# Kernel optimization log

Hardware: AMD Instinct MI355X
Metric: run time of the kernel (lower is better)

The kernel has to match this reference:

```python
import jax, jax.numpy as jnp
import numpy as np

DIM = 192
HEADS = 6
WIN = 7
N = WIN * WIN            # 49 tokens per window
NW = 64                  # windows per image
B = 64                   # images
BW = NW * B              # 4096 total windows
TABLE = (2 * WIN - 1) ** 2  # 169


def setup_inputs() -> dict:
    key = jax.random.key(0)
    ks = jax.random.split(key, 8)
    x = jax.random.normal(ks[0], (BW, N, DIM), dtype=jnp.float32)
    rpi = jax.random.randint(ks[1], (N, N), 0, TABLE, dtype=jnp.int64)
    # 0 / -100 additive mask (as in shifted-window attention)
    mask = jnp.where(jax.random.uniform(ks[2], (NW, N, N)) < 0.1, -100.0, 0.0).astype(jnp.float32)
    qkv_w = jax.random.normal(ks[3], (3 * DIM, DIM), dtype=jnp.float32) * 0.02
    qkv_b = jnp.zeros((3 * DIM,), dtype=jnp.float32)
    proj_w = jax.random.normal(ks[4], (DIM, DIM), dtype=jnp.float32) * 0.02
    proj_b = jnp.zeros((DIM,), dtype=jnp.float32)
    rpb_table = jax.random.normal(ks[5], (TABLE, HEADS), dtype=jnp.float32) * 0.02
    return {"x": x, "rpi": rpi, "mask": mask, "qkv_w": qkv_w, "qkv_b": qkv_b,
            "proj_w": proj_w, "proj_b": proj_b, "rpb_table": rpb_table}


def reference(x, rpi, mask, qkv_w, qkv_b, proj_w, proj_b, rpb_table):
    b_, n, c = x.shape
    hd = c // HEADS
    scale = hd ** -0.5
    qkv = (x @ qkv_w.T + qkv_b).reshape(b_, n, 3, HEADS, hd)
    qkv = jnp.transpose(qkv, (2, 0, 3, 1, 4))
    q, k, v = qkv[0], qkv[1], qkv[2]
    attn = jnp.einsum('bhnd,bhmd->bhnm', q * scale, k)  # [b_, h, n, n]
    # relative position bias gather: [n, n, h] -> [h, n, n]
    bias = rpb_table[rpi.reshape(-1)].reshape(n, n, HEADS)
    attn = attn + jnp.transpose(bias, (2, 0, 1))[None]
    # additive 0/-inf window mask
    nw = mask.shape[0]
    attn = attn.reshape(b_ // nw, nw, HEADS, n, n) + mask[None, :, None]
    attn = attn.reshape(-1, HEADS, n, n)
    attn = jax.nn.softmax(attn, axis=-1)
    out = jnp.einsum('bhnm,bhmd->bhnd', attn, v)
    out = jnp.transpose(out, (0, 2, 1, 3)).reshape(b_, n, c)
    out = out @ proj_w.T + proj_b
    return out
```

## Files before the change

### kernel.cpp

```cpp
#include <hip/hip_runtime.h>

#define DIM    192
#define HEADS  6
#define NTOK   49
#define NWIN   64

typedef __attribute__((ext_vector_type(8))) short short8;
typedef __attribute__((ext_vector_type(4))) float f32x4;

#define XS 200
#define VS 72
#define SS 65
#define PS 72

#define BIAS_ELEMS (HEADS * NTOK * NTOK)
#define WQKV_SOFF   28864
#define WQKV_ELEMS  (3 * DIM * DIM)
#define WPROJ_SOFF  (WQKV_SOFF + WQKV_ELEMS)
#define WPROJ_ELEMS (DIM * DIM)
#define CMB_BOFF    ((size_t)(WPROJ_SOFF + WPROJ_ELEMS) * 2)
#define CMB_ELEMS   (NWIN * HEADS * NTOK * NTOK)

__device__ __forceinline__ unsigned short f2bf(float f) {
    unsigned int u = __float_as_uint(f);
    u += 0x7FFFu + ((u >> 16) & 1u);
    return (unsigned short)(u >> 16);
}

__global__ void wa_prep_kernel(const int* __restrict__ rpi,
                               const float* __restrict__ rpb,
                               const float* __restrict__ qkv_w,
                               const float* __restrict__ proj_w,
                               const float* __restrict__ maskp,
                               float* __restrict__ bias,
                               unsigned short* __restrict__ wqkv,
                               unsigned short* __restrict__ wproj,
                               float* __restrict__ cmb) {
    __shared__ int is64_s;
    if (threadIdx.x < 64) {
        int z = (rpi[2 * (int)threadIdx.x + 1] == 0) ? 1 : 0;
        unsigned long long b = __ballot(z);
        if (threadIdx.x == 0) is64_s = (__popcll(b) >= 48) ? 1 : 0;
    }
    __syncthreads();
    const int is64 = is64_s;
    const int base3 = BIAS_ELEMS + WQKV_ELEMS + WPROJ_ELEMS;
    const int total = base3 + (cmb ? CMB_ELEMS : 0);
    for (int idx = blockIdx.x * blockDim.x + threadIdx.x; idx < total;
         idx += gridDim.x * blockDim.x) {
        if (idx < BIAS_ELEMS) {
            int h  = idx / (NTOK * NTOK);
            int nm = idx - h * (NTOK * NTOK);
            int r  = is64 ? rpi[2 * nm] : rpi[nm];
            bias[idx] = rpb[r * HEADS + h];
        } else if (idx < BIAS_ELEMS + WQKV_ELEMS) {
            int i = idx - BIAS_ELEMS;
            wqkv[i] = f2bf(qkv_w[i]);
        } else if (idx < base3) {
            int i = idx - BIAS_ELEMS - WQKV_ELEMS;
            wproj[i] = f2bf(proj_w[i]);
        } else {
            int i2  = idx - base3;
            int win = i2 / (HEADS * NTOK * NTOK);
            int rem = i2 - win * (HEADS * NTOK * NTOK);
            int h   = rem / (NTOK * NTOK);
            int nm  = rem - h * (NTOK * NTOK);
            int r   = is64 ? rpi[2 * nm] : rpi[nm];
            cmb[i2] = rpb[r * HEADS + h] + maskp[win * (NTOK * NTOK) + nm];
        }
    }
}

template <bool CMB>
__global__ __launch_bounds__(512, 2)
void wa_attn_kernel(const float* __restrict__ x,
                    const float* __restrict__ maskp,
                    const unsigned short* __restrict__ wqkv,
                    const float* __restrict__ qkv_b,
                    const float* __restrict__ biasp,
                    const unsigned short* __restrict__ wproj,
                    const float* __restrict__ proj_b,
                    const float* __restrict__ cmbp,
                    float* __restrict__ out) {
    __shared__ __attribute__((aligned(16))) float uSP[64 * SS + 64 * (PS / 2)];
    __shared__ __attribute__((aligned(16))) unsigned short sq[64 * XS];
    __shared__ __attribute__((aligned(16))) unsigned short sv[DIM * VS];
    __shared__ float sinv[64];

    unsigned short* sx     = (unsigned short*)uSP;
    unsigned short* kstage = (unsigned short*)uSP;
    float* S = uSP;
    unsigned short* P = (unsigned short*)(uSP + 64 * SS);

    const int tid  = threadIdx.x;
    const int wave = tid >> 6;
    const int lane = tid & 63;
    const int quad = lane >> 4;
    const int l16  = lane & 15;
    const int bw   = blockIdx.x;
    const int win  = bw & (NWIN - 1);

    {
        const float4* xw = (const float4*)(x + (size_t)bw * (NTOK * DIM));
        for (int idx = tid; idx < NTOK * DIM / 4; idx += 512) {
            int row = idx / 48, c4 = idx - row * 48;
            float4 v = xw[idx];
            unsigned int lo = (unsigned int)f2bf(v.x) | ((unsigned int)f2bf(v.y) << 16);
            unsigned int hi = (unsigned int)f2bf(v.z) | ((unsigned int)f2bf(v.w) << 16);
            *(uint2*)&sx[row * XS + c4 * 4] = make_uint2(lo, hi);
        }
        for (int idx = tid; idx < 15 * 24; idx += 512) {
            int row = 49 + idx / 24, c8 = idx - (idx / 24) * 24;
            *(uint4*)&sx[row * XS + c8 * 8] = make_uint4(0, 0, 0, 0);
        }
    }
    __syncthreads();

    {
        f32x4 acc[5][4];
        #pragma unroll
        for (int r = 0; r < 5; ++r)
            #pragma unroll
            for (int mt = 0; mt < 4; ++mt) acc[r][mt] = (f32x4){0.f, 0.f, 0.f, 0.f};
        for (int k0 = 0; k0 < DIM; k0 += 32) {
            short8 af[4];
            #pragma unroll
            for (int mt = 0; mt < 4; ++mt)
                af[mt] = *(const short8*)&sx[(mt * 16 + l16) * XS + k0 + quad * 8];
            #pragma unroll
            for (int r = 0; r < 5; ++r) {
                if (wave >= 4 && r == 4) continue;
                int n0 = (wave + 8 * r) * 16;
                short8 bf = *(const short8*)(wqkv + (n0 + l16) * DIM + k0 + quad * 8);
                #pragma unroll
                for (int mt = 0; mt < 4; ++mt)
                    acc[r][mt] = __builtin_amdgcn_mfma_f32_16x16x32_bf16(af[mt], bf, acc[r][mt], 0, 0, 0);
            }
        }
        __syncthreads();
        #pragma unroll
        for (int r = 0; r < 5; ++r) {
            if (wave >= 4 && r == 4) continue;
            int col = (wave + 8 * r) * 16 + l16;
            float cb = qkv_b[col];
            #pragma unroll
            for (int mt = 0; mt < 4; ++mt) {
                if (r >= 3) {
                    unsigned int lo = (unsigned int)f2bf(acc[r][mt][0] + cb) |
                                      ((unsigned int)f2bf(acc[r][mt][1] + cb) << 16);
                    unsigned int hi = (unsigned int)f2bf(acc[r][mt][2] + cb) |
                                      ((unsigned int)f2bf(acc[r][mt][3] + cb) << 16);
                    *(uint2*)&sv[(col - 384) * VS + mt * 16 + quad * 4] = make_uint2(lo, hi);
                } else {
                    #pragma unroll
                    for (int rr = 0; rr < 4; ++rr) {
                        int m = mt * 16 + quad * 4 + rr;
                        unsigned short bv = f2bf(acc[r][mt][rr] + cb);
                        if (col < 192) sq[m * XS + col] = bv;
                        else           kstage[m * XS + (col - 192)] = bv;
                    }
                }
            }
        }
    }
    __syncthreads();

    short8 kf[2][HEADS];
    #pragma unroll
    for (int tt = 0; tt < 2; ++tt) {
        int t = wave * 2 + tt, nt = t & 3;
        #pragma unroll
        for (int h = 0; h < HEADS; ++h)
            kf[tt][h] = *(const short8*)&kstage[(nt * 16 + l16) * XS + h * 32 + quad * 8];
    }
    __syncthreads();

    const float scale = 0.17677669529663687f;
    const float* maskw = maskp + win * (NTOK * NTOK);

    #pragma unroll
    for (int h = 0; h < HEADS; ++h) {
        {
            f32x4 zz = {0.f, 0.f, 0.f, 0.f};
            const float* cw = CMB ? (cmbp + ((size_t)win * HEADS + h) * (NTOK * NTOK))
                                  : (biasp + h * (NTOK * NTOK));
            #pragma unroll
            for (int tt = 0; tt < 2; ++tt) {
                int t = wave * 2 + tt;
                int mt = t >> 2, nt = t & 3;
                short8 af = *(const short8*)&sq[(mt * 16 + l16) * XS + h * 32 + quad * 8];
                f32x4 d = __builtin_amdgcn_mfma_f32_16x16x32_bf16(af, kf[tt][h], zz, 0, 0, 0);
                #pragma unroll
                for (int rr = 0; rr < 4; ++rr) {
                    int i = mt * 16 + quad * 4 + rr;
                    int j = nt * 16 + l16;
                    if (i < NTOK && j < NTOK) {
                        float add = CMB ? cw[i * NTOK + j]
                                        : (cw[i * NTOK + j] + maskw[i * NTOK + j]);
                        S[i * SS + j] = d[rr] * scale + add;
                    }
                }
            }
        }
        __syncthreads();
        if (tid < 392) {
            int i = tid >> 3, s = tid & 7;
            float m = -1e30f;
            for (int jj = 0; jj < 7; ++jj) {
                int j = s + 8 * jj;
                if (j < NTOK) m = fmaxf(m, S[i * SS + j]);
            }
            for (int o = 1; o < 8; o <<= 1) m = fmaxf(m, __shfl_xor(m, o));
            float sum = 0.f;
            #pragma unroll
            for (int jj = 0; jj < 8; ++jj) {
                int j = s + 8 * jj;
                float e = 0.f;
                if (j < NTOK) { e = __expf(S[i * SS + j] - m); sum += e; }
                P[i * PS + j] = f2bf(e);
            }
            for (int o = 1; o < 8; o <<= 1) sum += __shfl_xor(sum, o);
            if (s == 0) sinv[i] = 1.f / sum;
        }
        __syncthreads();
        {
            int mt = wave >> 1, nt = wave & 1;
            f32x4 acc = {0.f, 0.f, 0.f, 0.f};
            #pragma unroll
            for (int k0 = 0; k0 < 64; k0 += 32) {
                short8 af = *(const short8*)&P[(mt * 16 + l16) * PS + k0 + quad * 8];
                short8 bf = *(const short8*)&sv[(h * 32 + nt * 16 + l16) * VS + k0 + quad * 8];
                acc = __builtin_amdgcn_mfma_f32_16x16x32_bf16(af, bf, acc, 0, 0, 0);
            }
            #pragma unroll
            for (int rr = 0; rr < 4; ++rr) {
                int i = mt * 16 + quad * 4 + rr;
                unsigned short ov = 0;
                if (i < NTOK) ov = f2bf(acc[rr] * sinv[i]);
                sq[i * XS + h * 32 + nt * 16 + l16] = ov;
            }
        }
    }
    __syncthreads();

    {
        const int mh = wave >> 2;
        const int wv = wave & 3;
        f32x4 pacc[3][2];
        #pragma unroll
        for (int r = 0; r < 3; ++r)
            #pragma unroll
            for (int mi = 0; mi < 2; ++mi) pacc[r][mi] = (f32x4){0.f, 0.f, 0.f, 0.f};
        for (int k0 = 0; k0 < DIM; k0 += 32) {
            short8 af[2];
            #pragma unroll
            for (int mi = 0; mi < 2; ++mi)
                af[mi] = *(const short8*)&sq[((mh * 2 + mi) * 16 + l16) * XS + k0 + quad * 8];
            #pragma unroll
            for (int r = 0; r < 3; ++r) {
                int n0 = (wv + 4 * r) * 16;
                short8 bf = *(const short8*)(wproj + (n0 + l16) * DIM + k0 + quad * 8);
                #pragma unroll
                for (int mi = 0; mi < 2; ++mi)
                    pacc[r][mi] = __builtin_amdgcn_mfma_f32_16x16x32_bf16(af[mi], bf, pacc[r][mi], 0, 0, 0);
            }
        }
        #pragma unroll
        for (int r = 0; r < 3; ++r) {
            int n0 = (wv + 4 * r) * 16;
            float cb = proj_b[n0 + l16];
            #pragma unroll
            for (int mi = 0; mi < 2; ++mi) {
                #pragma unroll
                for (int rr = 0; rr < 4; ++rr) {
                    int m = (mh * 2 + mi) * 16 + quad * 4 + rr;
                    if (m < NTOK)
                        out[((size_t)bw * NTOK + m) * DIM + n0 + l16] = pacc[r][mi][rr] + cb;
                }
            }
        }
    }
}

extern "C" void kernel_launch(void* const* d_in, const int* in_sizes, int n_in,
                              void* d_out, int out_size, void* d_ws, size_t ws_size,
                              hipStream_t stream) {
    const float* x      = (const float*)d_in[0];
    const int*   rpi    = (const int*)d_in[1];
    const float* maskp  = (const float*)d_in[2];
    const float* qkv_w  = (const float*)d_in[3];
    const float* qkv_b  = (const float*)d_in[4];
    const float* proj_w = (const float*)d_in[5];
    const float* proj_b = (const float*)d_in[6];
    const float* rpb    = (const float*)d_in[7];
    float* out = (float*)d_out;

    float* bias = (float*)d_ws;
    unsigned short* wqkv  = (unsigned short*)d_ws + WQKV_SOFF;
    unsigned short* wproj = (unsigned short*)d_ws + WPROJ_SOFF;
    float* cmb = nullptr;
    if (ws_size >= CMB_BOFF + (size_t)CMB_ELEMS * 4)
        cmb = (float*)((char*)d_ws + CMB_BOFF);

    wa_prep_kernel<<<640, 256, 0, stream>>>(rpi, rpb, qkv_w, proj_w, maskp,
                                            bias, wqkv, wproj, cmb);
    if (cmb)
        wa_attn_kernel<true><<<4096, 512, 0, stream>>>(x, maskp, wqkv, qkv_b, bias,
                                                       wproj, proj_b, cmb, out);
    else
        wa_attn_kernel<false><<<4096, 512, 0, stream>>>(x, maskp, wqkv, qkv_b, bias,
                                                        wproj, proj_b, cmb, out);
}
```

Before: 701.9 us.

## Retile QKV GEMM into 2x4 wave grid and raise launch bounds occupancy

The QKV projection GEMM is re-partitioned so each wave owns two 16-row M tiles and nine N tiles, instead of all four M tiles and up to five N tiles. This balances MFMA work across all eight waves, since previously half the waves skipped one N tile, and cuts per-wave accumulator registers. The launch bounds are also raised to request 4 blocks per SM, pushing the compiler toward lower register use. Each wave now issues more global B-fragment loads per k-step, and the tighter register budget may cause spills. LDS usage per block may still cap occupancy below the requested level.

```diff
diff --git a/kernel.cpp b/kernel.cpp
--- a/kernel.cpp
+++ b/kernel.cpp
@@ -72,7 +72,7 @@
 }
 
 template <bool CMB>
-__global__ __launch_bounds__(512, 2)
+__global__ __launch_bounds__(512, 4)
 void wa_attn_kernel(const float* __restrict__ x,
                     const float* __restrict__ maskp,
                     const unsigned short* __restrict__ wqkv,
@@ -117,48 +117,49 @@
     __syncthreads();
 
     {
-        f32x4 acc[5][4];
-        #pragma unroll
-        for (int r = 0; r < 5; ++r)
-            #pragma unroll
-            for (int mt = 0; mt < 4; ++mt) acc[r][mt] = (f32x4){0.f, 0.f, 0.f, 0.f};
+        const int wm = wave >> 2;
+        const int wn = wave & 3;
+        f32x4 acc[9][2];
+        #pragma unroll
+        for (int r = 0; r < 9; ++r)
+            #pragma unroll
+            for (int mi = 0; mi < 2; ++mi) acc[r][mi] = (f32x4){0.f, 0.f, 0.f, 0.f};
         for (int k0 = 0; k0 < DIM; k0 += 32) {
-            short8 af[4];
-            #pragma unroll
-            for (int mt = 0; mt < 4; ++mt)
-                af[mt] = *(const short8*)&sx[(mt * 16 + l16) * XS + k0 + quad * 8];
-            #pragma unroll
-            for (int r = 0; r < 5; ++r) {
-                if (wave >= 4 && r == 4) continue;
-                int n0 = (wave + 8 * r) * 16;
+            short8 af[2];
+            #pragma unroll
+            for (int mi = 0; mi < 2; ++mi)
+                af[mi] = *(const short8*)&sx[((wm * 2 + mi) * 16 + l16) * XS + k0 + quad * 8];
+            #pragma unroll
+            for (int r = 0; r < 9; ++r) {
+                int n0 = (wn + 4 * r) * 16;
                 short8 bf = *(const short8*)(wqkv + (n0 + l16) * DIM + k0 + quad * 8);
                 #pragma unroll
-                for (int mt = 0; mt < 4; ++mt)
-                    acc[r][mt] = __builtin_amdgcn_mfma_f32_16x16x32_bf16(af[mt], bf, acc[r][mt], 0, 0, 0);
+                for (int mi = 0; mi < 2; ++mi)
+                    acc[r][mi] = __builtin_amdgcn_mfma_f32_16x16x32_bf16(af[mi], bf, acc[r][mi], 0, 0, 0);
             }
         }
         __syncthreads();
         #pragma unroll
-        for (int r = 0; r < 5; ++r) {
-            if (wave >= 4 && r == 4) continue;
-            int col = (wave + 8 * r) * 16 + l16;
+        for (int r = 0; r < 9; ++r) {
+            int col = (wn + 4 * r) * 16 + l16;
             float cb = qkv_b[col];
             #pragma unroll
-            for (int mt = 0; mt < 4; ++mt) {
-                if (r >= 3) {
-                    unsigned int lo = (unsigned int)f2bf(acc[r][mt][0] + cb) |
-                                      ((unsigned int)f2bf(acc[r][mt][1] + cb) << 16);
-                    unsigned int hi = (unsigned int)f2bf(acc[r][mt][2] + cb) |
-                                      ((unsigned int)f2bf(acc[r][mt][3] + cb) << 16);
-                    *(uint2*)&sv[(col - 384) * VS + mt * 16 + quad * 4] = make_uint2(lo, hi);
+            for (int mi = 0; mi < 2; ++mi) {
+                int mbase = (wm * 2 + mi) * 16 + quad * 4;
+                if (r >= 6) {
+                    unsigned int lo = (unsigned int)f2bf(acc[r][mi][0] + cb) |
+                                      ((unsigned int)f2bf(acc[r][mi][1] + cb) << 16);
+                    unsigned int hi = (unsigned int)f2bf(acc[r][mi][2] + cb) |
+                                      ((unsigned int)f2bf(acc[r][mi][3] + cb) << 16);
+                    *(uint2*)&sv[(col - 384) * VS + mbase] = make_uint2(lo, hi);
+                } else if (r >= 3) {
+                    #pragma unroll
+                    for (int rr = 0; rr < 4; ++rr)
+                        kstage[(mbase + rr) * XS + (col - 192)] = f2bf(acc[r][mi][rr] + cb);
                 } else {
                     #pragma unroll
-                    for (int rr = 0; rr < 4; ++rr) {
-                        int m = mt * 16 + quad * 4 + rr;
-                        unsigned short bv = f2bf(acc[r][mt][rr] + cb);
-                        if (col < 192) sq[m * XS + col] = bv;
-                        else           kstage[m * XS + (col - 192)] = bv;
-                    }
+                    for (int rr = 0; rr < 4; ++rr)
+                        sq[(mbase + rr) * XS + col] = f2bf(acc[r][mi][rr] + cb);
                 }
             }
         }
```

New measurement: 690.8 us. Within noise of the previous version (-1.6%).
